# Optimization experiments

Measured on AMD Instinct MI355X. Metric: run time of the kernel, lower is better.

Reference implementation:

```python
import jax, jax.numpy as jnp
import numpy as np

NEG_INF = -1e9


def setup_inputs() -> dict:
    key = jax.random.key(0)
    k1, k2, k3, k4 = jax.random.split(key, 4)
    B, S, D, P = 4, 256, 512, 256
    sequence = jax.random.normal(k1, (B, S, D), dtype=jnp.float32)
    sequence_mask = jnp.ones((B, S), dtype=jnp.float32)
    W1 = jax.random.normal(k2, (P, D), dtype=jnp.float32) * (1.0 / np.sqrt(D))
    W2 = jax.random.normal(k3, (P, D), dtype=jnp.float32) * (1.0 / np.sqrt(D))
    v = jax.random.normal(k4, (P,), dtype=jnp.float32) * (1.0 / np.sqrt(P))
    return {"sequence": sequence, "sequence_mask": sequence_mask,
            "W1": W1, "W2": W2, "v": v}


def reference(sequence, sequence_mask, W1, W2, v):
    # sequence: [B, S, D]; sequence_mask: [B, S] (1 = valid)
    # Projection (additive) self-attention, vectorized over all query positions.
    pk = jnp.einsum('bsd,pd->bsp', sequence, W1)  # key projections  [B, S, P]
    pq = jnp.einsum('bsd,pd->bsp', sequence, W2)  # query projections [B, S, P]
    # scores[b, i, j] = v . tanh(pq[b, i] + pk[b, j])   (i = query, j = key)
    scores = jnp.einsum('bijp,p->bij',
                        jnp.tanh(pq[:, :, None, :] + pk[:, None, :, :]), v)
    # mask keys, softmax over key dim
    key_mask = sequence_mask[:, None, :] > 0          # [B, 1, S]
    scores = jnp.where(key_mask, scores, NEG_INF)
    weights = jax.nn.softmax(scores, axis=-1)         # [B, Sq, Sk]
    attn = jnp.einsum('bij,bjd->bid', weights, sequence)  # [B, S, D]
    # mask_sequence: zero out invalid query positions
    attn = attn * sequence_mask[:, :, None]
    weights = weights * sequence_mask[:, :, None]
    return attn, weights
```

## Files before the change

kernel.cpp:

```cpp
#include <hip/hip_runtime.h>

constexpr int B = 4;
constexpr int S = 256;
constexpr int D = 512;
constexpr int P = 256;
constexpr float NEG_INF = -1e9f;
constexpr float LOG2E = 1.4426950408889634f;
constexpr float C2 = 2.885390081777927f;

__device__ __forceinline__ float fast_exp2(float x) {
#if __has_builtin(__builtin_amdgcn_exp2f)
    return __builtin_amdgcn_exp2f(x);
#else
    return exp2f(x);
#endif
}

__device__ __forceinline__ float fast_rcp(float x) {
#if __has_builtin(__builtin_amdgcn_rcpf)
    return __builtin_amdgcn_rcpf(x);
#else
    return 1.0f / x;
#endif
}

__global__ __launch_bounds__(256)
void proj_kernel(const float* __restrict__ seq,
                 const float* __restrict__ W1, const float* __restrict__ W2,
                 float* __restrict__ Eq, float* __restrict__ EkT) {
    __shared__ float As[64][34];
    __shared__ float Ws[64][68];

    int bid0 = blockIdx.x;
    int bid = (bid0 & 7) * 32 + (bid0 >> 3);

    const float* A;
    const float* Bp;
    float* out;
    if (bid < 128) {
        int mt = bid >> 2, nt = bid & 3;
        A = seq + (size_t)mt * 32 * D;
        Bp = W2 + (size_t)nt * 64 * D;
        out = Eq + (size_t)mt * 32 * 256 + nt * 64;
    } else {
        int r = bid - 128;
        int b = r >> 5, t = r & 31;
        int mt = t >> 2, nt = t & 3;
        A = W1 + (size_t)mt * 32 * D;
        Bp = seq + ((size_t)b * S + nt * 64) * D;
        out = EkT + (size_t)b * P * S + (size_t)mt * 32 * 256 + nt * 64;
    }

    int tid = threadIdx.x;
    int tx = tid & 15, ty = tid >> 4;
    int ar = tid >> 3, acg = tid & 7;
    int br = tid >> 2, bcg = tid & 3;
    const float* aptr = A + (size_t)ar * D + acg * 8;
    const float* bptr = Bp + (size_t)br * D + bcg * 16;

    float4 a0, a1, w0, w1, w2, w3;
    a0 = *(const float4*)(aptr);      a1 = *(const float4*)(aptr + 4);
    w0 = *(const float4*)(bptr);      w1 = *(const float4*)(bptr + 4);
    w2 = *(const float4*)(bptr + 8);  w3 = *(const float4*)(bptr + 12);

    float c0[4] = {0.f, 0.f, 0.f, 0.f};
    float c1[4] = {0.f, 0.f, 0.f, 0.f};

    for (int kt = 0; kt < 8; kt++) {
        int ka = acg * 8;
        As[ka + 0][ar] = a0.x; As[ka + 1][ar] = a0.y;
        As[ka + 2][ar] = a0.z; As[ka + 3][ar] = a0.w;
        As[ka + 4][ar] = a1.x; As[ka + 5][ar] = a1.y;
        As[ka + 6][ar] = a1.z; As[ka + 7][ar] = a1.w;
        int kb = bcg * 16;
        Ws[kb + 0][br] = w0.x;  Ws[kb + 1][br] = w0.y;
        Ws[kb + 2][br] = w0.z;  Ws[kb + 3][br] = w0.w;
        Ws[kb + 4][br] = w1.x;  Ws[kb + 5][br] = w1.y;
        Ws[kb + 6][br] = w1.z;  Ws[kb + 7][br] = w1.w;
        Ws[kb + 8][br] = w2.x;  Ws[kb + 9][br] = w2.y;
        Ws[kb + 10][br] = w2.z; Ws[kb + 11][br] = w2.w;
        Ws[kb + 12][br] = w3.x; Ws[kb + 13][br] = w3.y;
        Ws[kb + 14][br] = w3.z; Ws[kb + 15][br] = w3.w;
        __syncthreads();
        if (kt < 7) {
            const float* ap = aptr + (kt + 1) * 64;
            const float* bp = bptr + (kt + 1) * 64;
            a0 = *(const float4*)(ap);     a1 = *(const float4*)(ap + 4);
            w0 = *(const float4*)(bp);     w1 = *(const float4*)(bp + 4);
            w2 = *(const float4*)(bp + 8); w3 = *(const float4*)(bp + 12);
        }
#pragma unroll 8
        for (int k = 0; k < 64; k++) {
            float2 av = *(const float2*)&As[k][ty * 2];
            float4 wv = *(const float4*)&Ws[k][tx * 4];
            c0[0] = fmaf(av.x, wv.x, c0[0]);
            c0[1] = fmaf(av.x, wv.y, c0[1]);
            c0[2] = fmaf(av.x, wv.z, c0[2]);
            c0[3] = fmaf(av.x, wv.w, c0[3]);
            c1[0] = fmaf(av.y, wv.x, c1[0]);
            c1[1] = fmaf(av.y, wv.y, c1[1]);
            c1[2] = fmaf(av.y, wv.z, c1[2]);
            c1[3] = fmaf(av.y, wv.w, c1[3]);
        }
        __syncthreads();
    }
    float4 o0 = {fast_exp2(c0[0] * C2), fast_exp2(c0[1] * C2),
                 fast_exp2(c0[2] * C2), fast_exp2(c0[3] * C2)};
    float4 o1 = {fast_exp2(c1[0] * C2), fast_exp2(c1[1] * C2),
                 fast_exp2(c1[2] * C2), fast_exp2(c1[3] * C2)};
    *(float4*)&out[(size_t)(ty * 2 + 0) * 256 + tx * 4] = o0;
    *(float4*)&out[(size_t)(ty * 2 + 1) * 256 + tx * 4] = o1;
}

__global__ __launch_bounds__(512)
void score_attn_kernel(const float* __restrict__ seq,
                       const float* __restrict__ EkT, const float* __restrict__ Eq,
                       const float* __restrict__ v, const float* __restrict__ mask,
                       float* __restrict__ wout, float* __restrict__ attn) {
    __shared__ float Eqs[4][P];
    __shared__ float vs[P];
    __shared__ float part[4][4][S];
    __shared__ float wsm[S][4];
    __shared__ float redm[4][8], reds[4][8];

    int bid0 = blockIdx.x;
    int bid = (bid0 & 7) * 32 + (bid0 >> 3);
    int b = bid >> 6;
    int i0 = (bid & 63) * 4;
    int tid = threadIdx.x;
    int lane = tid & 63, wid = tid >> 6;

    ((float2*)Eqs)[tid] = ((const float2*)(Eq + ((size_t)b * S + i0) * P))[tid];
    if (tid < 128) {
        float2 vv = ((const float2*)v)[tid];
        ((float2*)vs)[tid] = make_float2(-2.f * vv.x, -2.f * vv.y);
    }
    __syncthreads();

    {
        int jg = tid & 127, h = tid >> 7;
        const float2* kp = (const float2*)(EkT + (size_t)b * P * S) + jg;
        int pbase = h * 64;
        float acc[2][4] = {{0.f, 0.f, 0.f, 0.f}, {0.f, 0.f, 0.f, 0.f}};
        for (int pp = 0; pp < 64; pp += 4) {
            int p = pbase + pp;
            float2 kk[4];
#pragma unroll
            for (int t = 0; t < 4; t++) kk[t] = kp[(size_t)(p + t) * 128];
            float4 vv4 = *(const float4*)&vs[p];
            float vvv[4] = {vv4.x, vv4.y, vv4.z, vv4.w};
#pragma unroll
            for (int q = 0; q < 4; q++) {
                float4 e4 = *(const float4*)&Eqs[q][p];
                float ee[4] = {e4.x, e4.y, e4.z, e4.w};
#pragma unroll
                for (int t = 0; t < 4; t++) {
                    float t0 = fmaf(kk[t].x, ee[t], 1.f);
                    float t1 = fmaf(kk[t].y, ee[t], 1.f);
                    acc[0][q] = fmaf(vvv[t], fast_rcp(t0), acc[0][q]);
                    acc[1][q] = fmaf(vvv[t], fast_rcp(t1), acc[1][q]);
                }
            }
        }
#pragma unroll
        for (int q = 0; q < 4; q++)
            ((float2*)&part[h][q][0])[jg] = make_float2(acc[0][q], acc[1][q]);
    }
    __syncthreads();

    float s[4], e[4] = {0.f, 0.f, 0.f, 0.f};
    if (tid < 256) {
        int j = tid;
        float km = mask[(size_t)b * S + j];
#pragma unroll
        for (int q = 0; q < 4; q++) {
            float sv = (part[0][q][j] + part[1][q][j]) +
                       (part[2][q][j] + part[3][q][j]);
            s[q] = (km > 0.f) ? sv : NEG_INF;
            float mm = s[q];
#pragma unroll
            for (int off = 32; off >= 1; off >>= 1)
                mm = fmaxf(mm, __shfl_xor(mm, off, 64));
            if (lane == 0) redm[q][wid] = mm;
        }
    }
    __syncthreads();
    if (tid < 256) {
#pragma unroll
        for (int q = 0; q < 4; q++) {
            float mm = fmaxf(fmaxf(redm[q][0], redm[q][1]),
                             fmaxf(redm[q][2], redm[q][3]));
            float ee = fast_exp2((s[q] - mm) * LOG2E);
            e[q] = ee;
            float ss = ee;
#pragma unroll
            for (int off = 32; off >= 1; off >>= 1)
                ss += __shfl_xor(ss, off, 64);
            if (lane == 0) reds[q][wid] = ss;
        }
    }
    __syncthreads();
    if (tid < 256) {
        int j = tid;
#pragma unroll
        for (int q = 0; q < 4; q++) {
            float ssum = (reds[q][0] + reds[q][1]) + (reds[q][2] + reds[q][3]);
            float qm = mask[(size_t)b * S + i0 + q];
            float w = e[q] * fast_rcp(ssum) * qm;
            wsm[j][q] = w;
            wout[((size_t)b * S + i0 + q) * S + j] = w;
        }
    }
    __syncthreads();

    {
        int d = tid;
        const float* sp = seq + (size_t)b * S * D + d;
        float a0 = 0.f, a1 = 0.f, a2 = 0.f, a3 = 0.f;
#pragma unroll 8
        for (int j = 0; j < S; j++) {
            float sv = sp[(size_t)j * D];
            float4 w4 = *(const float4*)&wsm[j][0];
            a0 = fmaf(w4.x, sv, a0);
            a1 = fmaf(w4.y, sv, a1);
            a2 = fmaf(w4.z, sv, a2);
            a3 = fmaf(w4.w, sv, a3);
        }
        attn[((size_t)b * S + i0 + 0) * D + d] = a0;
        attn[((size_t)b * S + i0 + 1) * D + d] = a1;
        attn[((size_t)b * S + i0 + 2) * D + d] = a2;
        attn[((size_t)b * S + i0 + 3) * D + d] = a3;
    }
}

extern "C" void kernel_launch(void* const* d_in, const int* in_sizes, int n_in,
                              void* d_out, int out_size, void* d_ws, size_t ws_size,
                              hipStream_t stream) {
    const float* seq  = (const float*)d_in[0];
    const float* mask = (const float*)d_in[1];
    const float* W1   = (const float*)d_in[2];
    const float* W2   = (const float*)d_in[3];
    const float* v    = (const float*)d_in[4];

    float* attn = (float*)d_out;
    float* wout = attn + (size_t)B * S * D;

    float* Eq  = (float*)d_ws;
    float* EkT = Eq + (size_t)B * S * P;

    proj_kernel<<<256, 256, 0, stream>>>(seq, W1, W2, Eq, EkT);
    score_attn_kernel<<<B * (S / 4), 512, 0, stream>>>(seq, EkT, Eq, v, mask,
                                                       wout, attn);
}
```

Before: 42.01 us.

## Double-buffer key projections in LDS and vectorize attn accumulation with split-j reduction

```diff
diff --git a/kernel.cpp b/kernel.cpp
--- a/kernel.cpp
+++ b/kernel.cpp
@@ -118,9 +118,11 @@
                        const float* __restrict__ v, const float* __restrict__ mask,
                        float* __restrict__ wout, float* __restrict__ attn) {
     __shared__ float Eqs[4][P];
-    __shared__ float vs[P];
-    __shared__ float part[4][4][S];
+    __shared__ float vsm[P];
+    __shared__ float ekb[2][32][256];
+    __shared__ float part[2][4][S];
     __shared__ float wsm[S][4];
+    __shared__ float p3[4][4][D];
     __shared__ float redm[4][8], reds[4][8];
 
     int bid0 = blockIdx.x;
@@ -130,52 +132,71 @@
     int tid = threadIdx.x;
     int lane = tid & 63, wid = tid >> 6;
 
+    const float* ekbase = EkT + (size_t)b * P * S;
+
+    float4 r0, r1, r2, r3;
+#define LOADC(c)                                                       \
+    {                                                                  \
+        const float4* sp_ = (const float4*)(ekbase + (c) * 8192);      \
+        r0 = sp_[tid]; r1 = sp_[tid + 512];                            \
+        r2 = sp_[tid + 1024]; r3 = sp_[tid + 1536];                    \
+    }
+#define WRITEC(bf)                                                     \
+    {                                                                  \
+        float4* dp_ = (float4*)&ekb[bf][0][0];                         \
+        dp_[tid] = r0; dp_[tid + 512] = r1;                            \
+        dp_[tid + 1024] = r2; dp_[tid + 1536] = r3;                    \
+    }
+
+    LOADC(0);
     ((float2*)Eqs)[tid] = ((const float2*)(Eq + ((size_t)b * S + i0) * P))[tid];
     if (tid < 128) {
         float2 vv = ((const float2*)v)[tid];
-        ((float2*)vs)[tid] = make_float2(-2.f * vv.x, -2.f * vv.y);
-    }
-    __syncthreads();
-
-    {
-        int jg = tid & 127, h = tid >> 7;
-        const float2* kp = (const float2*)(EkT + (size_t)b * P * S) + jg;
-        int pbase = h * 64;
-        float acc[2][4] = {{0.f, 0.f, 0.f, 0.f}, {0.f, 0.f, 0.f, 0.f}};
-        for (int pp = 0; pp < 64; pp += 4) {
-            int p = pbase + pp;
-            float2 kk[4];
-#pragma unroll
-            for (int t = 0; t < 4; t++) kk[t] = kp[(size_t)(p + t) * 128];
-            float4 vv4 = *(const float4*)&vs[p];
-            float vvv[4] = {vv4.x, vv4.y, vv4.z, vv4.w};
+        ((float2*)vsm)[tid] = make_float2(-2.f * vv.x, -2.f * vv.y);
+    }
+    WRITEC(0);
+    LOADC(1);
+    __syncthreads();
+
+    int j = tid & 255, h = tid >> 8;
+    float acc[4] = {0.f, 0.f, 0.f, 0.f};
+    for (int c = 0; c < 8; c++) {
+        int cur = c & 1;
+        int pl0 = h * 16;
+        int pg0 = c * 32 + pl0;
+#pragma unroll
+        for (int t = 0; t < 4; t++) {
+            int pl = pl0 + t * 4, pg = pg0 + t * 4;
+            float e0 = ekb[cur][pl + 0][j];
+            float e1 = ekb[cur][pl + 1][j];
+            float e2 = ekb[cur][pl + 2][j];
+            float e3 = ekb[cur][pl + 3][j];
+            float4 vv = *(const float4*)&vsm[pg];
 #pragma unroll
             for (int q = 0; q < 4; q++) {
-                float4 e4 = *(const float4*)&Eqs[q][p];
-                float ee[4] = {e4.x, e4.y, e4.z, e4.w};
-#pragma unroll
-                for (int t = 0; t < 4; t++) {
-                    float t0 = fmaf(kk[t].x, ee[t], 1.f);
-                    float t1 = fmaf(kk[t].y, ee[t], 1.f);
-                    acc[0][q] = fmaf(vvv[t], fast_rcp(t0), acc[0][q]);
-                    acc[1][q] = fmaf(vvv[t], fast_rcp(t1), acc[1][q]);
-                }
+                float4 eq = *(const float4*)&Eqs[q][pg];
+                acc[q] = fmaf(vv.x, fast_rcp(fmaf(e0, eq.x, 1.f)), acc[q]);
+                acc[q] = fmaf(vv.y, fast_rcp(fmaf(e1, eq.y, 1.f)), acc[q]);
+                acc[q] = fmaf(vv.z, fast_rcp(fmaf(e2, eq.z, 1.f)), acc[q]);
+                acc[q] = fmaf(vv.w, fast_rcp(fmaf(e3, eq.w, 1.f)), acc[q]);
             }
         }
-#pragma unroll
-        for (int q = 0; q < 4; q++)
-            ((float2*)&part[h][q][0])[jg] = make_float2(acc[0][q], acc[1][q]);
-    }
+        if (c < 7) { WRITEC(cur ^ 1); }
+        if (c < 6) { LOADC(c + 2); }
+        __syncthreads();
+    }
+#undef LOADC
+#undef WRITEC
+#pragma unroll
+    for (int q = 0; q < 4; q++) part[h][q][j] = acc[q];
     __syncthreads();
 
     float s[4], e[4] = {0.f, 0.f, 0.f, 0.f};
     if (tid < 256) {
-        int j = tid;
         float km = mask[(size_t)b * S + j];
 #pragma unroll
         for (int q = 0; q < 4; q++) {
-            float sv = (part[0][q][j] + part[1][q][j]) +
-                       (part[2][q][j] + part[3][q][j]);
+            float sv = part[0][q][j] + part[1][q][j];
             s[q] = (km > 0.f) ? sv : NEG_INF;
             float mm = s[q];
 #pragma unroll
@@ -201,7 +222,6 @@
     }
     __syncthreads();
     if (tid < 256) {
-        int j = tid;
 #pragma unroll
         for (int q = 0; q < 4; q++) {
             float ssum = (reds[q][0] + reds[q][1]) + (reds[q][2] + reds[q][3]);
@@ -214,22 +234,38 @@
     __syncthreads();
 
     {
+        int dg = tid & 127, jh = tid >> 7;
+        int d0 = dg * 4;
+        const float4* sp = (const float4*)(seq + (size_t)b * S * D);
+        float4 A0 = {0.f, 0.f, 0.f, 0.f}, A1 = {0.f, 0.f, 0.f, 0.f};
+        float4 A2 = {0.f, 0.f, 0.f, 0.f}, A3 = {0.f, 0.f, 0.f, 0.f};
+#pragma unroll 4
+        for (int jj = 0; jj < 64; jj++) {
+            int jx = jh * 64 + jj;
+            float4 s4 = sp[(size_t)jx * 128 + dg];
+            float4 w4 = *(const float4*)&wsm[jx][0];
+            A0.x = fmaf(w4.x, s4.x, A0.x); A0.y = fmaf(w4.x, s4.y, A0.y);
+            A0.z = fmaf(w4.x, s4.z, A0.z); A0.w = fmaf(w4.x, s4.w, A0.w);
+            A1.x = fmaf(w4.y, s4.x, A1.x); A1.y = fmaf(w4.y, s4.y, A1.y);
+            A1.z = fmaf(w4.y, s4.z, A1.z); A1.w = fmaf(w4.y, s4.w, A1.w);
+            A2.x = fmaf(w4.z, s4.x, A2.x); A2.y = fmaf(w4.z, s4.y, A2.y);
+            A2.z = fmaf(w4.z, s4.z, A2.z); A2.w = fmaf(w4.z, s4.w, A2.w);
+            A3.x = fmaf(w4.w, s4.x, A3.x); A3.y = fmaf(w4.w, s4.y, A3.y);
+            A3.z = fmaf(w4.w, s4.z, A3.z); A3.w = fmaf(w4.w, s4.w, A3.w);
+        }
+        *(float4*)&p3[jh][0][d0] = A0;
+        *(float4*)&p3[jh][1][d0] = A1;
+        *(float4*)&p3[jh][2][d0] = A2;
+        *(float4*)&p3[jh][3][d0] = A3;
+    }
+    __syncthreads();
+    {
         int d = tid;
-        const float* sp = seq + (size_t)b * S * D + d;
-        float a0 = 0.f, a1 = 0.f, a2 = 0.f, a3 = 0.f;
-#pragma unroll 8
-        for (int j = 0; j < S; j++) {
-            float sv = sp[(size_t)j * D];
-            float4 w4 = *(const float4*)&wsm[j][0];
-            a0 = fmaf(w4.x, sv, a0);
-            a1 = fmaf(w4.y, sv, a1);
-            a2 = fmaf(w4.z, sv, a2);
-            a3 = fmaf(w4.w, sv, a3);
-        }
-        attn[((size_t)b * S + i0 + 0) * D + d] = a0;
-        attn[((size_t)b * S + i0 + 1) * D + d] = a1;
-        attn[((size_t)b * S + i0 + 2) * D + d] = a2;
-        attn[((size_t)b * S + i0 + 3) * D + d] = a3;
+#pragma unroll
+        for (int q = 0; q < 4; q++) {
+            float r = (p3[0][q][d] + p3[1][q][d]) + (p3[2][q][d] + p3[3][q][d]);
+            attn[((size_t)b * S + i0 + q) * D + d] = r;
+        }
     }
 }
 
```

Result: no change. 41.29 us (-1.7%).

## Split fused score/attention kernel into separate score and attention kernels

Applied to the files above, without the earlier changes.

```diff
diff --git a/kernel.cpp b/kernel.cpp
--- a/kernel.cpp
+++ b/kernel.cpp
@@ -113,124 +113,126 @@
 }
 
 __global__ __launch_bounds__(512)
-void score_attn_kernel(const float* __restrict__ seq,
-                       const float* __restrict__ EkT, const float* __restrict__ Eq,
-                       const float* __restrict__ v, const float* __restrict__ mask,
-                       float* __restrict__ wout, float* __restrict__ attn) {
-    __shared__ float Eqs[4][P];
-    __shared__ float vs[P];
-    __shared__ float part[4][4][S];
-    __shared__ float wsm[S][4];
-    __shared__ float redm[4][8], reds[4][8];
-
-    int bid0 = blockIdx.x;
-    int bid = (bid0 & 7) * 32 + (bid0 >> 3);
-    int b = bid >> 6;
-    int i0 = (bid & 63) * 4;
+void score_kernel(const float* __restrict__ EkT, const float* __restrict__ Eq,
+                  const float* __restrict__ v, const float* __restrict__ mask,
+                  float* __restrict__ wout) {
+    __shared__ float Eqs[2][P];
+    __shared__ float vsm[P];
+    __shared__ float part[2][2][S];
+    __shared__ float redm[2][4], reds[2][4];
+
+    int b0 = blockIdx.x;
+    int bid = (b0 & 7) * 64 + (b0 >> 3);
+    int b = bid >> 7;
+    int i0 = (bid & 127) * 2;
     int tid = threadIdx.x;
+    int j = tid & 255, h = tid >> 8;
+
+    ((float*)Eqs)[tid] = Eq[((size_t)b * S + i0) * P + tid];
+    if (tid < 256) vsm[tid] = -2.f * v[tid];
+    __syncthreads();
+
+    {
+        const float* ekp = EkT + ((size_t)b * P + h * 128) * S + j;
+        float a0 = 0.f, a1 = 0.f;
+        int pb = h * 128;
+#pragma unroll 8
+        for (int pp = 0; pp < 128; ++pp) {
+            float ek = ekp[(size_t)pp * S];
+            int p = pb + pp;
+            float vv = vsm[p];
+            float e0 = Eqs[0][p], e1 = Eqs[1][p];
+            a0 = fmaf(vv, fast_rcp(fmaf(ek, e0, 1.f)), a0);
+            a1 = fmaf(vv, fast_rcp(fmaf(ek, e1, 1.f)), a1);
+        }
+        part[h][0][j] = a0;
+        part[h][1][j] = a1;
+    }
+    __syncthreads();
+
     int lane = tid & 63, wid = tid >> 6;
-
-    ((float2*)Eqs)[tid] = ((const float2*)(Eq + ((size_t)b * S + i0) * P))[tid];
-    if (tid < 128) {
-        float2 vv = ((const float2*)v)[tid];
-        ((float2*)vs)[tid] = make_float2(-2.f * vv.x, -2.f * vv.y);
-    }
-    __syncthreads();
+    float s0 = 0.f, s1 = 0.f, e0 = 0.f, e1 = 0.f;
+    if (tid < 256) {
+        float km = mask[(size_t)b * S + j];
+        s0 = part[0][0][j] + part[1][0][j];
+        s1 = part[0][1][j] + part[1][1][j];
+        if (!(km > 0.f)) { s0 = NEG_INF; s1 = NEG_INF; }
+        float m0 = s0, m1 = s1;
+#pragma unroll
+        for (int off = 32; off >= 1; off >>= 1) {
+            m0 = fmaxf(m0, __shfl_xor(m0, off, 64));
+            m1 = fmaxf(m1, __shfl_xor(m1, off, 64));
+        }
+        if (lane == 0) { redm[0][wid] = m0; redm[1][wid] = m1; }
+    }
+    __syncthreads();
+    if (tid < 256) {
+        float m0 = fmaxf(fmaxf(redm[0][0], redm[0][1]),
+                         fmaxf(redm[0][2], redm[0][3]));
+        float m1 = fmaxf(fmaxf(redm[1][0], redm[1][1]),
+                         fmaxf(redm[1][2], redm[1][3]));
+        e0 = fast_exp2((s0 - m0) * LOG2E);
+        e1 = fast_exp2((s1 - m1) * LOG2E);
+        float t0 = e0, t1 = e1;
+#pragma unroll
+        for (int off = 32; off >= 1; off >>= 1) {
+            t0 += __shfl_xor(t0, off, 64);
+            t1 += __shfl_xor(t1, off, 64);
+        }
+        if (lane == 0) { reds[0][wid] = t0; reds[1][wid] = t1; }
+    }
+    __syncthreads();
+    if (tid < 256) {
+        float sum0 = (reds[0][0] + reds[0][1]) + (reds[0][2] + reds[0][3]);
+        float sum1 = (reds[1][0] + reds[1][1]) + (reds[1][2] + reds[1][3]);
+        float qm0 = mask[(size_t)b * S + i0];
+        float qm1 = mask[(size_t)b * S + i0 + 1];
+        float w0 = e0 * fast_rcp(sum0) * qm0;
+        float w1 = e1 * fast_rcp(sum1) * qm1;
+        wout[((size_t)b * S + i0 + 0) * S + j] = w0;
+        wout[((size_t)b * S + i0 + 1) * S + j] = w1;
+    }
+}
+
+__global__ __launch_bounds__(256)
+void attn_kernel(const float* __restrict__ wout, const float* __restrict__ seq,
+                 float* __restrict__ attn) {
+    __shared__ float wsm[S][8];
+    int b0 = blockIdx.x;
+    int bid = (b0 & 7) * 32 + (b0 >> 3);
+    int ig8 = bid >> 1;
+    int dt = bid & 1;
+    int i0g = ig8 * 8;
+    int b = i0g >> 8;
+    int d0 = dt * 256;
+    int tid = threadIdx.x;
 
     {
-        int jg = tid & 127, h = tid >> 7;
-        const float2* kp = (const float2*)(EkT + (size_t)b * P * S) + jg;
-        int pbase = h * 64;
-        float acc[2][4] = {{0.f, 0.f, 0.f, 0.f}, {0.f, 0.f, 0.f, 0.f}};
-        for (int pp = 0; pp < 64; pp += 4) {
-            int p = pbase + pp;
-            float2 kk[4];
-#pragma unroll
-            for (int t = 0; t < 4; t++) kk[t] = kp[(size_t)(p + t) * 128];
-            float4 vv4 = *(const float4*)&vs[p];
-            float vvv[4] = {vv4.x, vv4.y, vv4.z, vv4.w};
-#pragma unroll
-            for (int q = 0; q < 4; q++) {
-                float4 e4 = *(const float4*)&Eqs[q][p];
-                float ee[4] = {e4.x, e4.y, e4.z, e4.w};
-#pragma unroll
-                for (int t = 0; t < 4; t++) {
-                    float t0 = fmaf(kk[t].x, ee[t], 1.f);
-                    float t1 = fmaf(kk[t].y, ee[t], 1.f);
-                    acc[0][q] = fmaf(vvv[t], fast_rcp(t0), acc[0][q]);
-                    acc[1][q] = fmaf(vvv[t], fast_rcp(t1), acc[1][q]);
-                }
-            }
-        }
-#pragma unroll
-        for (int q = 0; q < 4; q++)
-            ((float2*)&part[h][q][0])[jg] = make_float2(acc[0][q], acc[1][q]);
-    }
-    __syncthreads();
-
-    float s[4], e[4] = {0.f, 0.f, 0.f, 0.f};
-    if (tid < 256) {
-        int j = tid;
-        float km = mask[(size_t)b * S + j];
-#pragma unroll
-        for (int q = 0; q < 4; q++) {
-            float sv = (part[0][q][j] + part[1][q][j]) +
-                       (part[2][q][j] + part[3][q][j]);
-            s[q] = (km > 0.f) ? sv : NEG_INF;
-            float mm = s[q];
-#pragma unroll
-            for (int off = 32; off >= 1; off >>= 1)
-                mm = fmaxf(mm, __shfl_xor(mm, off, 64));
-            if (lane == 0) redm[q][wid] = mm;
-        }
-    }
-    __syncthreads();
-    if (tid < 256) {
-#pragma unroll
-        for (int q = 0; q < 4; q++) {
-            float mm = fmaxf(fmaxf(redm[q][0], redm[q][1]),
-                             fmaxf(redm[q][2], redm[q][3]));
-            float ee = fast_exp2((s[q] - mm) * LOG2E);
-            e[q] = ee;
-            float ss = ee;
-#pragma unroll
-            for (int off = 32; off >= 1; off >>= 1)
-                ss += __shfl_xor(ss, off, 64);
-            if (lane == 0) reds[q][wid] = ss;
-        }
-    }
-    __syncthreads();
-    if (tid < 256) {
-        int j = tid;
-#pragma unroll
-        for (int q = 0; q < 4; q++) {
-            float ssum = (reds[q][0] + reds[q][1]) + (reds[q][2] + reds[q][3]);
-            float qm = mask[(size_t)b * S + i0 + q];
-            float w = e[q] * fast_rcp(ssum) * qm;
-            wsm[j][q] = w;
-            wout[((size_t)b * S + i0 + q) * S + j] = w;
-        }
-    }
-    __syncthreads();
-
-    {
-        int d = tid;
-        const float* sp = seq + (size_t)b * S * D + d;
-        float a0 = 0.f, a1 = 0.f, a2 = 0.f, a3 = 0.f;
+        const float* wp = wout + (size_t)i0g * S + tid;
+#pragma unroll
+        for (int q = 0; q < 8; q++) wsm[tid][q] = wp[(size_t)q * S];
+    }
+    __syncthreads();
+
+    const float* sp = seq + (size_t)b * S * D + d0 + tid;
+    float acc[8] = {0.f, 0.f, 0.f, 0.f, 0.f, 0.f, 0.f, 0.f};
 #pragma unroll 8
-        for (int j = 0; j < S; j++) {
-            float sv = sp[(size_t)j * D];
-            float4 w4 = *(const float4*)&wsm[j][0];
-            a0 = fmaf(w4.x, sv, a0);
-            a1 = fmaf(w4.y, sv, a1);
-            a2 = fmaf(w4.z, sv, a2);
-            a3 = fmaf(w4.w, sv, a3);
-        }
-        attn[((size_t)b * S + i0 + 0) * D + d] = a0;
-        attn[((size_t)b * S + i0 + 1) * D + d] = a1;
-        attn[((size_t)b * S + i0 + 2) * D + d] = a2;
-        attn[((size_t)b * S + i0 + 3) * D + d] = a3;
-    }
+    for (int j = 0; j < S; ++j) {
+        float sv = sp[(size_t)j * D];
+        float4 wa = *(const float4*)&wsm[j][0];
+        float4 wb = *(const float4*)&wsm[j][4];
+        acc[0] = fmaf(wa.x, sv, acc[0]);
+        acc[1] = fmaf(wa.y, sv, acc[1]);
+        acc[2] = fmaf(wa.z, sv, acc[2]);
+        acc[3] = fmaf(wa.w, sv, acc[3]);
+        acc[4] = fmaf(wb.x, sv, acc[4]);
+        acc[5] = fmaf(wb.y, sv, acc[5]);
+        acc[6] = fmaf(wb.z, sv, acc[6]);
+        acc[7] = fmaf(wb.w, sv, acc[7]);
+    }
+    float* op = attn + (size_t)i0g * D + d0 + tid;
+#pragma unroll
+    for (int q = 0; q < 8; q++) op[(size_t)q * D] = acc[q];
 }
 
 extern "C" void kernel_launch(void* const* d_in, const int* in_sizes, int n_in,
@@ -249,6 +251,6 @@
     float* EkT = Eq + (size_t)B * S * P;
 
     proj_kernel<<<256, 256, 0, stream>>>(seq, W1, W2, Eq, EkT);
-    score_attn_kernel<<<B * (S / 4), 512, 0, stream>>>(seq, EkT, Eq, v, mask,
-                                                       wout, attn);
-}
+    score_kernel<<<512, 512, 0, stream>>>(EkT, Eq, v, mask, wout);
+    attn_kernel<<<256, 256, 0, stream>>>(wout, seq, attn);
+}
```

Measured after the change: 41.82 us. About the same (-0.5%).

## Double proj threads and restructure score loop split over two P halves

Applied to the files above, without the earlier changes.

```diff
diff --git a/kernel.cpp b/kernel.cpp
--- a/kernel.cpp
+++ b/kernel.cpp
@@ -24,7 +24,7 @@
 #endif
 }
 
-__global__ __launch_bounds__(256)
+__global__ __launch_bounds__(512)
 void proj_kernel(const float* __restrict__ seq,
                  const float* __restrict__ W1, const float* __restrict__ W2,
                  float* __restrict__ Eq, float* __restrict__ EkT) {
@@ -53,63 +53,49 @@
 
     int tid = threadIdx.x;
     int tx = tid & 15, ty = tid >> 4;
-    int ar = tid >> 3, acg = tid & 7;
-    int br = tid >> 2, bcg = tid & 3;
-    const float* aptr = A + (size_t)ar * D + acg * 8;
-    const float* bptr = Bp + (size_t)br * D + bcg * 16;
-
-    float4 a0, a1, w0, w1, w2, w3;
-    a0 = *(const float4*)(aptr);      a1 = *(const float4*)(aptr + 4);
-    w0 = *(const float4*)(bptr);      w1 = *(const float4*)(bptr + 4);
-    w2 = *(const float4*)(bptr + 8);  w3 = *(const float4*)(bptr + 12);
+    int ar = tid >> 4, akc = tid & 15;
+    int br = tid >> 3, bkc = tid & 7;
+    const float* aptr = A + (size_t)ar * D + akc * 4;
+    const float* bptr = Bp + (size_t)br * D + bkc * 8;
+
+    float4 a0, w0, w1;
+    a0 = *(const float4*)(aptr);
+    w0 = *(const float4*)(bptr);
+    w1 = *(const float4*)(bptr + 4);
 
     float c0[4] = {0.f, 0.f, 0.f, 0.f};
-    float c1[4] = {0.f, 0.f, 0.f, 0.f};
 
     for (int kt = 0; kt < 8; kt++) {
-        int ka = acg * 8;
+        int ka = akc * 4;
         As[ka + 0][ar] = a0.x; As[ka + 1][ar] = a0.y;
         As[ka + 2][ar] = a0.z; As[ka + 3][ar] = a0.w;
-        As[ka + 4][ar] = a1.x; As[ka + 5][ar] = a1.y;
-        As[ka + 6][ar] = a1.z; As[ka + 7][ar] = a1.w;
-        int kb = bcg * 16;
-        Ws[kb + 0][br] = w0.x;  Ws[kb + 1][br] = w0.y;
-        Ws[kb + 2][br] = w0.z;  Ws[kb + 3][br] = w0.w;
-        Ws[kb + 4][br] = w1.x;  Ws[kb + 5][br] = w1.y;
-        Ws[kb + 6][br] = w1.z;  Ws[kb + 7][br] = w1.w;
-        Ws[kb + 8][br] = w2.x;  Ws[kb + 9][br] = w2.y;
-        Ws[kb + 10][br] = w2.z; Ws[kb + 11][br] = w2.w;
-        Ws[kb + 12][br] = w3.x; Ws[kb + 13][br] = w3.y;
-        Ws[kb + 14][br] = w3.z; Ws[kb + 15][br] = w3.w;
+        int kb = bkc * 8;
+        Ws[kb + 0][br] = w0.x; Ws[kb + 1][br] = w0.y;
+        Ws[kb + 2][br] = w0.z; Ws[kb + 3][br] = w0.w;
+        Ws[kb + 4][br] = w1.x; Ws[kb + 5][br] = w1.y;
+        Ws[kb + 6][br] = w1.z; Ws[kb + 7][br] = w1.w;
         __syncthreads();
         if (kt < 7) {
             const float* ap = aptr + (kt + 1) * 64;
             const float* bp = bptr + (kt + 1) * 64;
-            a0 = *(const float4*)(ap);     a1 = *(const float4*)(ap + 4);
-            w0 = *(const float4*)(bp);     w1 = *(const float4*)(bp + 4);
-            w2 = *(const float4*)(bp + 8); w3 = *(const float4*)(bp + 12);
+            a0 = *(const float4*)(ap);
+            w0 = *(const float4*)(bp);
+            w1 = *(const float4*)(bp + 4);
         }
 #pragma unroll 8
         for (int k = 0; k < 64; k++) {
-            float2 av = *(const float2*)&As[k][ty * 2];
+            float av = As[k][ty];
             float4 wv = *(const float4*)&Ws[k][tx * 4];
-            c0[0] = fmaf(av.x, wv.x, c0[0]);
-            c0[1] = fmaf(av.x, wv.y, c0[1]);
-            c0[2] = fmaf(av.x, wv.z, c0[2]);
-            c0[3] = fmaf(av.x, wv.w, c0[3]);
-            c1[0] = fmaf(av.y, wv.x, c1[0]);
-            c1[1] = fmaf(av.y, wv.y, c1[1]);
-            c1[2] = fmaf(av.y, wv.z, c1[2]);
-            c1[3] = fmaf(av.y, wv.w, c1[3]);
+            c0[0] = fmaf(av, wv.x, c0[0]);
+            c0[1] = fmaf(av, wv.y, c0[1]);
+            c0[2] = fmaf(av, wv.z, c0[2]);
+            c0[3] = fmaf(av, wv.w, c0[3]);
         }
         __syncthreads();
     }
     float4 o0 = {fast_exp2(c0[0] * C2), fast_exp2(c0[1] * C2),
                  fast_exp2(c0[2] * C2), fast_exp2(c0[3] * C2)};
-    float4 o1 = {fast_exp2(c1[0] * C2), fast_exp2(c1[1] * C2),
-                 fast_exp2(c1[2] * C2), fast_exp2(c1[3] * C2)};
-    *(float4*)&out[(size_t)(ty * 2 + 0) * 256 + tx * 4] = o0;
-    *(float4*)&out[(size_t)(ty * 2 + 1) * 256 + tx * 4] = o1;
+    *(float4*)&out[(size_t)ty * 256 + tx * 4] = o0;
 }
 
 __global__ __launch_bounds__(512)
@@ -117,66 +103,60 @@
                        const float* __restrict__ EkT, const float* __restrict__ Eq,
                        const float* __restrict__ v, const float* __restrict__ mask,
                        float* __restrict__ wout, float* __restrict__ attn) {
-    __shared__ float Eqs[4][P];
-    __shared__ float vs[P];
-    __shared__ float part[4][4][S];
+    __shared__ float Eqs[P][4];
+    __shared__ float vsm[P];
+    __shared__ float part[2][S][4];
     __shared__ float wsm[S][4];
-    __shared__ float redm[4][8], reds[4][8];
+    __shared__ float redm[4][4], reds[4][4];
 
     int bid0 = blockIdx.x;
     int bid = (bid0 & 7) * 32 + (bid0 >> 3);
     int b = bid >> 6;
     int i0 = (bid & 63) * 4;
     int tid = threadIdx.x;
+
+    if (tid < 256) {
+        int p = tid;
+        float e0 = Eq[((size_t)b * S + i0 + 0) * P + p];
+        float e1 = Eq[((size_t)b * S + i0 + 1) * P + p];
+        float e2 = Eq[((size_t)b * S + i0 + 2) * P + p];
+        float e3 = Eq[((size_t)b * S + i0 + 3) * P + p];
+        *(float4*)&Eqs[p][0] = make_float4(e0, e1, e2, e3);
+        vsm[p] = -2.f * v[p];
+    }
+    __syncthreads();
+
+    int j = tid & 255, h = tid >> 8;
+    {
+        const float* ekp = EkT + ((size_t)b * P + h * 128) * S + j;
+        float a0 = 0.f, a1 = 0.f, a2 = 0.f, a3 = 0.f;
+#pragma unroll 8
+        for (int pp = 0; pp < 128; ++pp) {
+            float ek = ekp[(size_t)pp * S];
+            int p = h * 128 + pp;
+            float4 eq = *(const float4*)&Eqs[p][0];
+            float vv = vsm[p];
+            a0 = fmaf(vv, fast_rcp(fmaf(ek, eq.x, 1.f)), a0);
+            a1 = fmaf(vv, fast_rcp(fmaf(ek, eq.y, 1.f)), a1);
+            a2 = fmaf(vv, fast_rcp(fmaf(ek, eq.z, 1.f)), a2);
+            a3 = fmaf(vv, fast_rcp(fmaf(ek, eq.w, 1.f)), a3);
+        }
+        *(float4*)&part[h][j][0] = make_float4(a0, a1, a2, a3);
+    }
+    __syncthreads();
+
     int lane = tid & 63, wid = tid >> 6;
-
-    ((float2*)Eqs)[tid] = ((const float2*)(Eq + ((size_t)b * S + i0) * P))[tid];
-    if (tid < 128) {
-        float2 vv = ((const float2*)v)[tid];
-        ((float2*)vs)[tid] = make_float2(-2.f * vv.x, -2.f * vv.y);
-    }
-    __syncthreads();
-
-    {
-        int jg = tid & 127, h = tid >> 7;
-        const float2* kp = (const float2*)(EkT + (size_t)b * P * S) + jg;
-        int pbase = h * 64;
-        float acc[2][4] = {{0.f, 0.f, 0.f, 0.f}, {0.f, 0.f, 0.f, 0.f}};
-        for (int pp = 0; pp < 64; pp += 4) {
-            int p = pbase + pp;
-            float2 kk[4];
-#pragma unroll
-            for (int t = 0; t < 4; t++) kk[t] = kp[(size_t)(p + t) * 128];
-            float4 vv4 = *(const float4*)&vs[p];
-            float vvv[4] = {vv4.x, vv4.y, vv4.z, vv4.w};
-#pragma unroll
-            for (int q = 0; q < 4; q++) {
-                float4 e4 = *(const float4*)&Eqs[q][p];
-                float ee[4] = {e4.x, e4.y, e4.z, e4.w};
-#pragma unroll
-                for (int t = 0; t < 4; t++) {
-                    float t0 = fmaf(kk[t].x, ee[t], 1.f);
-                    float t1 = fmaf(kk[t].y, ee[t], 1.f);
-                    acc[0][q] = fmaf(vvv[t], fast_rcp(t0), acc[0][q]);
-                    acc[1][q] = fmaf(vvv[t], fast_rcp(t1), acc[1][q]);
-                }
-            }
-        }
-#pragma unroll
-        for (int q = 0; q < 4; q++)
-            ((float2*)&part[h][q][0])[jg] = make_float2(acc[0][q], acc[1][q]);
-    }
-    __syncthreads();
-
     float s[4], e[4] = {0.f, 0.f, 0.f, 0.f};
     if (tid < 256) {
-        int j = tid;
         float km = mask[(size_t)b * S + j];
+        float4 p0 = *(const float4*)&part[0][j][0];
+        float4 p1 = *(const float4*)&part[1][j][0];
+        s[0] = p0.x + p1.x; s[1] = p0.y + p1.y;
+        s[2] = p0.z + p1.z; s[3] = p0.w + p1.w;
+        if (!(km > 0.f)) { s[0] = NEG_INF; s[1] = NEG_INF;
+                           s[2] = NEG_INF; s[3] = NEG_INF; }
 #pragma unroll
         for (int q = 0; q < 4; q++) {
-            float sv = (part[0][q][j] + part[1][q][j]) +
-                       (part[2][q][j] + part[3][q][j]);
-            s[q] = (km > 0.f) ? sv : NEG_INF;
             float mm = s[q];
 #pragma unroll
             for (int off = 32; off >= 1; off >>= 1)
@@ -201,35 +181,35 @@
     }
     __syncthreads();
     if (tid < 256) {
-        int j = tid;
+        float w4[4];
 #pragma unroll
         for (int q = 0; q < 4; q++) {
             float ssum = (reds[q][0] + reds[q][1]) + (reds[q][2] + reds[q][3]);
             float qm = mask[(size_t)b * S + i0 + q];
-            float w = e[q] * fast_rcp(ssum) * qm;
-            wsm[j][q] = w;
-            wout[((size_t)b * S + i0 + q) * S + j] = w;
-        }
+            w4[q] = e[q] * fast_rcp(ssum) * qm;
+            wout[((size_t)b * S + i0 + q) * S + j] = w4[q];
+        }
+        *(float4*)&wsm[j][0] = make_float4(w4[0], w4[1], w4[2], w4[3]);
     }
     __syncthreads();
 
     {
         int d = tid;
         const float* sp = seq + (size_t)b * S * D + d;
-        float a0 = 0.f, a1 = 0.f, a2 = 0.f, a3 = 0.f;
+        float A0 = 0.f, A1 = 0.f, A2 = 0.f, A3 = 0.f;
 #pragma unroll 8
-        for (int j = 0; j < S; j++) {
-            float sv = sp[(size_t)j * D];
-            float4 w4 = *(const float4*)&wsm[j][0];
-            a0 = fmaf(w4.x, sv, a0);
-            a1 = fmaf(w4.y, sv, a1);
-            a2 = fmaf(w4.z, sv, a2);
-            a3 = fmaf(w4.w, sv, a3);
-        }
-        attn[((size_t)b * S + i0 + 0) * D + d] = a0;
-        attn[((size_t)b * S + i0 + 1) * D + d] = a1;
-        attn[((size_t)b * S + i0 + 2) * D + d] = a2;
-        attn[((size_t)b * S + i0 + 3) * D + d] = a3;
+        for (int jj = 0; jj < S; ++jj) {
+            float sv = sp[(size_t)jj * D];
+            float4 wv = *(const float4*)&wsm[jj][0];
+            A0 = fmaf(wv.x, sv, A0);
+            A1 = fmaf(wv.y, sv, A1);
+            A2 = fmaf(wv.z, sv, A2);
+            A3 = fmaf(wv.w, sv, A3);
+        }
+        attn[((size_t)b * S + i0 + 0) * D + d] = A0;
+        attn[((size_t)b * S + i0 + 1) * D + d] = A1;
+        attn[((size_t)b * S + i0 + 2) * D + d] = A2;
+        attn[((size_t)b * S + i0 + 3) * D + d] = A3;
     }
 }
 
@@ -248,7 +228,7 @@
     float* Eq  = (float*)d_ws;
     float* EkT = Eq + (size_t)B * S * P;
 
-    proj_kernel<<<256, 256, 0, stream>>>(seq, W1, W2, Eq, EkT);
-    score_attn_kernel<<<B * (S / 4), 512, 0, stream>>>(seq, EkT, Eq, v, mask,
-                                                       wout, attn);
-}
+    proj_kernel<<<256, 512, 0, stream>>>(seq, W1, W2, Eq, EkT);
+    score_attn_kernel<<<256, 512, 0, stream>>>(seq, EkT, Eq, v, mask,
+                                               wout, attn);
+}
```

Result: slower. 49.54 us (+17.9%).
